# Kernel tuning notes

Measured on AMD Instinct MI355X. Metric: run time of the kernel, lower is better.

## Reference

```python
import jax, jax.numpy as jnp
import numpy as np

WINDOW = 128  # causal window width
D_SCALE = None  # set from val dim at trace time


def _softsign(x):
    return x / (1.0 + jnp.abs(x))


def setup_inputs() -> dict:
    key = jax.random.key(0)
    k1, k2 = jax.random.split(key)
    B, N, D = 4, 4096, 256
    val = jax.random.normal(k1, (B, N, D), dtype=jnp.float32)
    state = jax.random.normal(k2, (B, N), dtype=jnp.float32)
    return {"val": val, "state": state}


def reference(val, state):
    # val: [B, N, D], state: [B, N]
    B, N, D = val.shape
    # pairwise_fn: scaled dot product -> scores [B, N, N]
    scores = jnp.einsum('bnd,bmd->bnm', val, val) / jnp.sqrt(jnp.asarray(D, val.dtype))
    # edge_compress_fn: softsign
    edges = _softsign(scores)
    # causal window mask: source j satisfies (j <= i) & (j >= i - window)
    i = jnp.arange(N)[:, None]
    j = jnp.arange(N)[None, :]
    mask = (j <= i) & (j >= i - WINDOW)  # [N, N]
    edges = edges * mask[None, :, :].astype(edges.dtype)
    # val_proj_fn / state_proj_fn are Identity
    delta_state = jnp.einsum('bij,bj->bi', edges, state)   # [B, N]
    delta_val = jnp.einsum('bij,bjd->bid', edges, val)      # [B, N, D]
    return (delta_state, delta_val)
```

## Files before the change

### kernel.cpp

```cpp
#include <hip/hip_runtime.h>

#define NSEQ 4096
#define DIM  256
#define WIN  128
#define BATCH 4

typedef __bf16 bf16x8 __attribute__((ext_vector_type(8)));
typedef float  f32x4  __attribute__((ext_vector_type(4)));
typedef int    v2i    __attribute__((ext_vector_type(2)));
typedef int    v4i    __attribute__((ext_vector_type(4)));

__device__ __forceinline__ int sub_off(int j, int d) {
    return (((j >> 2) * 16 + (d >> 4)) << 6) + ((j & 3) << 4) + (d & 15);
}

__device__ __forceinline__ unsigned short f2bf(float f) {
    unsigned u = __builtin_bit_cast(unsigned, f);
    u += 0x7fffu + ((u >> 16) & 1u);
    return (unsigned short)(u >> 16);
}

__device__ __forceinline__ unsigned pk2bf(float lo, float hi) {
    unsigned r;
    asm("v_cvt_pk_bf16_f32 %0, %1, %2" : "=v"(r) : "v"(lo), "v"(hi));
    return r;
}

__global__ __launch_bounds__(256, 3)
void sp_kernel(const float* __restrict__ val,
               const float* __restrict__ state,
               float* __restrict__ out) {
    __shared__ __align__(128) unsigned short vbuf[2][8192];
    __shared__ __align__(128) unsigned short E_s[32 * 56];
    __shared__ float ds_part[4][16];

    const int bx  = blockIdx.x;
    const int lbx = ((bx & 7) << 6) + (bx >> 3);
    const int b      = lbx >> 7;
    const int tile_i = lbx & 127;
    const int r0     = tile_i << 5;

    const int t   = threadIdx.x;
    const int w   = t >> 6;
    const int l   = t & 63;
    const int l15 = l & 15;
    const int l4  = l >> 4;
    const int mt  = w >> 1;
    const int jt  = w & 1;

    const float* valb = val + ((size_t)b * NSEQ) * DIM;
    const float* stb  = state + ((size_t)b * NSEQ);
    float* out_state  = out + ((size_t)b * NSEQ);
    float* out_val    = out + (size_t)BATCH * NSEQ + ((size_t)b * NSEQ) * DIM;

    const int s_jl0 = (w << 2) + l4;
    const int s_jl1 = s_jl0 + 16;

    {
        const float* src = valb + ((size_t)tile_i << 13);
        #pragma unroll
        for (int qq = 0; qq < 8; ++qq) {
            const int jl = (qq & 1) ? s_jl1 : s_jl0;
            const int d0 = (l15 << 2) + ((qq >> 1) << 6);
            float4 v = *reinterpret_cast<const float4*>(src + jl * DIM + d0);
            uint2 u;
            u.x = pk2bf(v.x, v.y);
            u.y = pk2bf(v.z, v.w);
            *reinterpret_cast<uint2*>(&vbuf[0][sub_off(jl, d0)]) = u;
        }
    }
    __syncthreads();

    const int il = (mt << 4) + l15;
    const int jl = (jt << 4) + l15;
    bf16x8 af[8];
    #pragma unroll
    for (int ks = 0; ks < 8; ++ks)
        af[ks] = *reinterpret_cast<const bf16x8*>(&vbuf[0][sub_off(il, (l4 << 3) + (ks << 5))]);

    const int tj0   = (tile_i >= 4) ? (tile_i - 4) : 0;
    const int ntile = tile_i - tj0 + 1;

    float dsacc[4] = {0.f, 0.f, 0.f, 0.f};
    f32x4 accpv[2][4];
    #pragma unroll
    for (int m2 = 0; m2 < 2; ++m2)
        #pragma unroll
        for (int tt = 0; tt < 4; ++tt)
            accpv[m2][tt] = (f32x4){0.f, 0.f, 0.f, 0.f};

    int p = 0;
    for (int q = 0; q < ntile; ++q) {
        const int ti = tile_i - q;
        const bool havenext = (q + 1 < ntile);
        const unsigned short* bp = &vbuf[p][0];
        unsigned short* bn = &vbuf[1 - p][0];

        const int jg = (ti << 5) + jl;
        const float stv = stb[jg];

        bf16x8 sb[8];
        #pragma unroll
        for (int ks = 0; ks < 8; ++ks)
            sb[ks] = *reinterpret_cast<const bf16x8*>(&bp[sub_off(jl, (l4 << 3) + (ks << 5))]);
        f32x4 acc = (f32x4){0.f, 0.f, 0.f, 0.f};
        __builtin_amdgcn_s_setprio(1);
        #pragma unroll
        for (int ks = 0; ks < 8; ++ks)
            acc = __builtin_amdgcn_mfma_f32_16x16x32_bf16(af[ks], sb[ks], acc, 0, 0, 0);
        __builtin_amdgcn_s_setprio(0);

        const int ib = r0 + (mt << 4) + (l4 << 2);
        #pragma unroll
        for (int r = 0; r < 4; ++r) {
            float s = acc[r] * 0.0625f;
            float e = s * __builtin_amdgcn_rcpf(1.0f + fabsf(s));
            const int ig = ib + r;
            if (jg > ig || jg < ig - WIN) e = 0.0f;
            dsacc[r] += e * stv;
            E_s[((mt << 4) + (l4 << 2) + r) * 56 + (jt << 4) + l15] = f2bf(e);
        }

        if (havenext) {
            const float* src = valb + ((size_t)(ti - 1) << 13);
            #pragma unroll
            for (int qq = 0; qq < 8; ++qq) {
                const int jl2 = (qq & 1) ? s_jl1 : s_jl0;
                const int d0  = (l15 << 2) + ((qq >> 1) << 6);
                float4 v = *reinterpret_cast<const float4*>(src + jl2 * DIM + d0);
                uint2 u;
                u.x = pk2bf(v.x, v.y);
                u.y = pk2bf(v.z, v.w);
                *reinterpret_cast<uint2*>(&bn[sub_off(jl2, d0)]) = u;
            }
        }
        __syncthreads();

        bf16x8 ef0 = *reinterpret_cast<const bf16x8*>(&E_s[l15 * 56 + (l4 << 3)]);
        bf16x8 ef1 = *reinterpret_cast<const bf16x8*>(&E_s[(16 + l15) * 56 + (l4 << 3)]);
        const unsigned lds_base = (unsigned)(size_t)bp;
        v2i tr[8];
        #pragma unroll
        for (int tt = 0; tt < 4; ++tt) {
            const int nt = (w << 2) + tt;
            unsigned a0 = lds_base + (unsigned)((((l4 << 5) + nt) << 7) + (l15 << 3));
            asm volatile("ds_read_b64_tr_b16 %0, %1" : "=v"(tr[2 * tt]) : "v"(a0) : "memory");
            asm volatile("ds_read_b64_tr_b16 %0, %1 offset:2048" : "=v"(tr[2 * tt + 1]) : "v"(a0) : "memory");
        }
        asm volatile("s_waitcnt lgkmcnt(0)" ::: "memory");
        __builtin_amdgcn_sched_barrier(0);
        __builtin_amdgcn_s_setprio(1);
        #pragma unroll
        for (int tt = 0; tt < 4; ++tt) {
            v4i tmp;
            tmp.x = tr[2 * tt].x;     tmp.y = tr[2 * tt].y;
            tmp.z = tr[2 * tt + 1].x; tmp.w = tr[2 * tt + 1].y;
            bf16x8 bfr = __builtin_bit_cast(bf16x8, tmp);
            accpv[0][tt] = __builtin_amdgcn_mfma_f32_16x16x32_bf16(ef0, bfr, accpv[0][tt], 0, 0, 0);
            accpv[1][tt] = __builtin_amdgcn_mfma_f32_16x16x32_bf16(ef1, bfr, accpv[1][tt], 0, 0, 0);
        }
        __builtin_amdgcn_s_setprio(0);
        if (havenext) __syncthreads();
        p ^= 1;
    }

    #pragma unroll
    for (int m = 1; m <= 8; m <<= 1) {
        #pragma unroll
        for (int r = 0; r < 4; ++r)
            dsacc[r] += __shfl_xor(dsacc[r], m, 64);
    }
    if (l15 == 0) {
        #pragma unroll
        for (int r = 0; r < 4; ++r)
            ds_part[w][(l4 << 2) + r] = dsacc[r];
    }
    __syncthreads();
    if (t < 32) {
        const int m2 = t >> 4;
        out_state[r0 + t] = ds_part[(m2 << 1)][t & 15] + ds_part[(m2 << 1) + 1][t & 15];
    }

    #pragma unroll
    for (int m2 = 0; m2 < 2; ++m2) {
        #pragma unroll
        for (int tt = 0; tt < 4; ++tt) {
            const int d = (w << 6) + (tt << 4) + l15;
            #pragma unroll
            for (int r = 0; r < 4; ++r) {
                const int ig = r0 + (m2 << 4) + (l4 << 2) + r;
                out_val[(size_t)ig * DIM + d] = accpv[m2][tt][r];
            }
        }
    }
}

extern "C" void kernel_launch(void* const* d_in, const int* in_sizes, int n_in,
                              void* d_out, int out_size, void* d_ws, size_t ws_size,
                              hipStream_t stream) {
    const float* val   = (const float*)d_in[0];
    const float* state = (const float*)d_in[1];
    float* out = (float*)d_out;
    sp_kernel<<<dim3(BATCH * (NSEQ / 32)), dim3(256), 0, stream>>>(val, state, out);
}
```

Before: 16.53 us.

## Process 64-column source tiles per iteration and load query fragments directly from global

The key/value source tile grows from 32 to 64 rows, aligned to 64, so each iteration computes two score MFMAs per wave and two PV k-slices. This halves the number of loop iterations and barriers. The query A-fragments are now built straight from global memory instead of going through LDS. The cost is doubled LDS per block, occupancy dropping from 3 to 2 blocks, and some wasted fully masked columns from the coarser alignment.

```diff
diff --git a/kernel.cpp b/kernel.cpp
--- a/kernel.cpp
+++ b/kernel.cpp
@@ -26,12 +26,14 @@
     return r;
 }
 
-__global__ __launch_bounds__(256, 3)
+#define ESTR 72
+
+__global__ __launch_bounds__(256, 2)
 void sp_kernel(const float* __restrict__ val,
                const float* __restrict__ state,
                float* __restrict__ out) {
-    __shared__ __align__(128) unsigned short vbuf[2][8192];
-    __shared__ __align__(128) unsigned short E_s[32 * 56];
+    __shared__ __align__(128) unsigned short vbuf[2][16384];
+    __shared__ __align__(128) unsigned short E_s[32 * ESTR];
     __shared__ float ds_part[4][16];
 
     const int bx  = blockIdx.x;
@@ -53,33 +55,45 @@
     float* out_state  = out + ((size_t)b * NSEQ);
     float* out_val    = out + (size_t)BATCH * NSEQ + ((size_t)b * NSEQ) * DIM;
 
-    const int s_jl0 = (w << 2) + l4;
-    const int s_jl1 = s_jl0 + 16;
-
+    const int il = (mt << 4) + l15;
+    bf16x8 af[8];
     {
-        const float* src = valb + ((size_t)tile_i << 13);
-        #pragma unroll
-        for (int qq = 0; qq < 8; ++qq) {
-            const int jl = (qq & 1) ? s_jl1 : s_jl0;
-            const int d0 = (l15 << 2) + ((qq >> 1) << 6);
-            float4 v = *reinterpret_cast<const float4*>(src + jl * DIM + d0);
-            uint2 u;
-            u.x = pk2bf(v.x, v.y);
-            u.y = pk2bf(v.z, v.w);
-            *reinterpret_cast<uint2*>(&vbuf[0][sub_off(jl, d0)]) = u;
-        }
+        const float* rp = valb + (size_t)(r0 + il) * DIM + (l4 << 3);
+        #pragma unroll
+        for (int ks = 0; ks < 8; ++ks) {
+            float4 u0 = *reinterpret_cast<const float4*>(rp + (ks << 5));
+            float4 u1 = *reinterpret_cast<const float4*>(rp + (ks << 5) + 4);
+            v4i pw;
+            pw.x = pk2bf(u0.x, u0.y);
+            pw.y = pk2bf(u0.z, u0.w);
+            pw.z = pk2bf(u1.x, u1.y);
+            pw.w = pk2bf(u1.z, u1.w);
+            af[ks] = __builtin_bit_cast(bf16x8, pw);
+        }
+    }
+
+    const int jb0   = (r0 >= WIN) ? ((r0 - WIN) & ~63) : 0;
+    const int niter = (((r0 + 95) & ~63) - jb0) >> 6;
+
+    const int sj = (w << 2) + l4;
+    const int sd = l15 << 2;
+
+    {
+        const float* src = valb + (size_t)jb0 * DIM;
+        #pragma unroll
+        for (int a = 0; a < 4; ++a)
+            #pragma unroll
+            for (int c = 0; c < 4; ++c) {
+                const int jl = sj + (a << 4);
+                const int d0 = sd + (c << 6);
+                float4 v = *reinterpret_cast<const float4*>(src + jl * DIM + d0);
+                uint2 u;
+                u.x = pk2bf(v.x, v.y);
+                u.y = pk2bf(v.z, v.w);
+                *reinterpret_cast<uint2*>(&vbuf[0][sub_off(jl, d0)]) = u;
+            }
     }
     __syncthreads();
-
-    const int il = (mt << 4) + l15;
-    const int jl = (jt << 4) + l15;
-    bf16x8 af[8];
-    #pragma unroll
-    for (int ks = 0; ks < 8; ++ks)
-        af[ks] = *reinterpret_cast<const bf16x8*>(&vbuf[0][sub_off(il, (l4 << 3) + (ks << 5))]);
-
-    const int tj0   = (tile_i >= 4) ? (tile_i - 4) : 0;
-    const int ntile = tile_i - tj0 + 1;
 
     float dsacc[4] = {0.f, 0.f, 0.f, 0.f};
     f32x4 accpv[2][4];
@@ -89,79 +103,92 @@
         for (int tt = 0; tt < 4; ++tt)
             accpv[m2][tt] = (f32x4){0.f, 0.f, 0.f, 0.f};
 
-    int p = 0;
-    for (int q = 0; q < ntile; ++q) {
-        const int ti = tile_i - q;
-        const bool havenext = (q + 1 < ntile);
-        const unsigned short* bp = &vbuf[p][0];
-        unsigned short* bn = &vbuf[1 - p][0];
-
-        const int jg = (ti << 5) + jl;
-        const float stv = stb[jg];
-
-        bf16x8 sb[8];
-        #pragma unroll
-        for (int ks = 0; ks < 8; ++ks)
-            sb[ks] = *reinterpret_cast<const bf16x8*>(&bp[sub_off(jl, (l4 << 3) + (ks << 5))]);
-        f32x4 acc = (f32x4){0.f, 0.f, 0.f, 0.f};
-        __builtin_amdgcn_s_setprio(1);
-        #pragma unroll
-        for (int ks = 0; ks < 8; ++ks)
-            acc = __builtin_amdgcn_mfma_f32_16x16x32_bf16(af[ks], sb[ks], acc, 0, 0, 0);
-        __builtin_amdgcn_s_setprio(0);
-
-        const int ib = r0 + (mt << 4) + (l4 << 2);
-        #pragma unroll
-        for (int r = 0; r < 4; ++r) {
-            float s = acc[r] * 0.0625f;
-            float e = s * __builtin_amdgcn_rcpf(1.0f + fabsf(s));
-            const int ig = ib + r;
-            if (jg > ig || jg < ig - WIN) e = 0.0f;
-            dsacc[r] += e * stv;
-            E_s[((mt << 4) + (l4 << 2) + r) * 56 + (jt << 4) + l15] = f2bf(e);
+    for (int q = 0; q < niter; ++q) {
+        const int jb = jb0 + (q << 6);
+        const bool havenext = (q + 1 < niter);
+        const unsigned short* bp = &vbuf[q & 1][0];
+        unsigned short* bn = &vbuf[(q + 1) & 1][0];
+
+        f32x4 acc0 = (f32x4){0.f, 0.f, 0.f, 0.f};
+        f32x4 acc1 = (f32x4){0.f, 0.f, 0.f, 0.f};
+        {
+            const int jc0 = (jt << 5) + l15;
+            const int jc1 = jc0 + 16;
+            #pragma unroll
+            for (int ks = 0; ks < 8; ++ks) {
+                const int k = (l4 << 3) + (ks << 5);
+                bf16x8 s0 = *reinterpret_cast<const bf16x8*>(&bp[sub_off(jc0, k)]);
+                bf16x8 s1 = *reinterpret_cast<const bf16x8*>(&bp[sub_off(jc1, k)]);
+                acc0 = __builtin_amdgcn_mfma_f32_16x16x32_bf16(af[ks], s0, acc0, 0, 0, 0);
+                acc1 = __builtin_amdgcn_mfma_f32_16x16x32_bf16(af[ks], s1, acc1, 0, 0, 0);
+            }
+        }
+
+        {
+            const int jg0 = jb + (jt << 5) + l15;
+            const int jg1 = jg0 + 16;
+            const float stv0 = stb[jg0];
+            const float stv1 = stb[jg1];
+            const int ib = r0 + (mt << 4) + (l4 << 2);
+            #pragma unroll
+            for (int r = 0; r < 4; ++r) {
+                const int ig = ib + r;
+                const int irow = (mt << 4) + (l4 << 2) + r;
+                float s0 = acc0[r] * 0.0625f;
+                float e0 = s0 * __builtin_amdgcn_rcpf(1.0f + fabsf(s0));
+                if (jg0 > ig || jg0 < ig - WIN) e0 = 0.0f;
+                float s1 = acc1[r] * 0.0625f;
+                float e1 = s1 * __builtin_amdgcn_rcpf(1.0f + fabsf(s1));
+                if (jg1 > ig || jg1 < ig - WIN) e1 = 0.0f;
+                dsacc[r] += e0 * stv0 + e1 * stv1;
+                E_s[irow * ESTR + (jt << 5) + l15]      = f2bf(e0);
+                E_s[irow * ESTR + (jt << 5) + 16 + l15] = f2bf(e1);
+            }
         }
 
         if (havenext) {
-            const float* src = valb + ((size_t)(ti - 1) << 13);
-            #pragma unroll
-            for (int qq = 0; qq < 8; ++qq) {
-                const int jl2 = (qq & 1) ? s_jl1 : s_jl0;
-                const int d0  = (l15 << 2) + ((qq >> 1) << 6);
-                float4 v = *reinterpret_cast<const float4*>(src + jl2 * DIM + d0);
-                uint2 u;
-                u.x = pk2bf(v.x, v.y);
-                u.y = pk2bf(v.z, v.w);
-                *reinterpret_cast<uint2*>(&bn[sub_off(jl2, d0)]) = u;
-            }
+            const float* src = valb + (size_t)(jb + 64) * DIM;
+            #pragma unroll
+            for (int a = 0; a < 4; ++a)
+                #pragma unroll
+                for (int c = 0; c < 4; ++c) {
+                    const int jl = sj + (a << 4);
+                    const int d0 = sd + (c << 6);
+                    float4 v = *reinterpret_cast<const float4*>(src + jl * DIM + d0);
+                    uint2 u;
+                    u.x = pk2bf(v.x, v.y);
+                    u.y = pk2bf(v.z, v.w);
+                    *reinterpret_cast<uint2*>(&bn[sub_off(jl, d0)]) = u;
+                }
         }
         __syncthreads();
 
-        bf16x8 ef0 = *reinterpret_cast<const bf16x8*>(&E_s[l15 * 56 + (l4 << 3)]);
-        bf16x8 ef1 = *reinterpret_cast<const bf16x8*>(&E_s[(16 + l15) * 56 + (l4 << 3)]);
-        const unsigned lds_base = (unsigned)(size_t)bp;
-        v2i tr[8];
-        #pragma unroll
-        for (int tt = 0; tt < 4; ++tt) {
-            const int nt = (w << 2) + tt;
-            unsigned a0 = lds_base + (unsigned)((((l4 << 5) + nt) << 7) + (l15 << 3));
-            asm volatile("ds_read_b64_tr_b16 %0, %1" : "=v"(tr[2 * tt]) : "v"(a0) : "memory");
-            asm volatile("ds_read_b64_tr_b16 %0, %1 offset:2048" : "=v"(tr[2 * tt + 1]) : "v"(a0) : "memory");
-        }
-        asm volatile("s_waitcnt lgkmcnt(0)" ::: "memory");
-        __builtin_amdgcn_sched_barrier(0);
-        __builtin_amdgcn_s_setprio(1);
-        #pragma unroll
-        for (int tt = 0; tt < 4; ++tt) {
-            v4i tmp;
-            tmp.x = tr[2 * tt].x;     tmp.y = tr[2 * tt].y;
-            tmp.z = tr[2 * tt + 1].x; tmp.w = tr[2 * tt + 1].y;
-            bf16x8 bfr = __builtin_bit_cast(bf16x8, tmp);
-            accpv[0][tt] = __builtin_amdgcn_mfma_f32_16x16x32_bf16(ef0, bfr, accpv[0][tt], 0, 0, 0);
-            accpv[1][tt] = __builtin_amdgcn_mfma_f32_16x16x32_bf16(ef1, bfr, accpv[1][tt], 0, 0, 0);
-        }
-        __builtin_amdgcn_s_setprio(0);
+        #pragma unroll
+        for (int kf = 0; kf < 2; ++kf) {
+            bf16x8 ef0 = *reinterpret_cast<const bf16x8*>(&E_s[l15 * ESTR + (kf << 5) + (l4 << 3)]);
+            bf16x8 ef1 = *reinterpret_cast<const bf16x8*>(&E_s[(16 + l15) * ESTR + (kf << 5) + (l4 << 3)]);
+            const unsigned lds_base = (unsigned)(size_t)bp + (unsigned)(kf << 14);
+            v2i tr[8];
+            #pragma unroll
+            for (int tt = 0; tt < 4; ++tt) {
+                const int nt = (w << 2) + tt;
+                unsigned a0 = lds_base + (unsigned)((l4 << 12) + (nt << 7) + (l15 << 3));
+                asm volatile("ds_read_b64_tr_b16 %0, %1" : "=v"(tr[2 * tt]) : "v"(a0) : "memory");
+                asm volatile("ds_read_b64_tr_b16 %0, %1 offset:2048" : "=v"(tr[2 * tt + 1]) : "v"(a0) : "memory");
+            }
+            asm volatile("s_waitcnt lgkmcnt(0)" ::: "memory");
+            __builtin_amdgcn_sched_barrier(0);
+            #pragma unroll
+            for (int tt = 0; tt < 4; ++tt) {
+                v4i tmp;
+                tmp.x = tr[2 * tt].x;     tmp.y = tr[2 * tt].y;
+                tmp.z = tr[2 * tt + 1].x; tmp.w = tr[2 * tt + 1].y;
+                bf16x8 bfr = __builtin_bit_cast(bf16x8, tmp);
+                accpv[0][tt] = __builtin_amdgcn_mfma_f32_16x16x32_bf16(ef0, bfr, accpv[0][tt], 0, 0, 0);
+                accpv[1][tt] = __builtin_amdgcn_mfma_f32_16x16x32_bf16(ef1, bfr, accpv[1][tt], 0, 0, 0);
+            }
+        }
         if (havenext) __syncthreads();
-        p ^= 1;
     }
 
     #pragma unroll
```

Result: slower. 21.01 us (+27.1%).
